# Kernel optimization log

Hardware: AMD Instinct MI355X
Metric: run time of the kernel (lower is better)

## Reference

```python
import jax, jax.numpy as jnp
import numpy as np

T = 1.0  # temperature

def _free_energy(v, W, b, c):
    # v: [B, V]; W: [V, H]; b: [V]; c: [H]
    vW = v @ W                                  # [B, H]
    W_colsum = W.sum(axis=0)                    # [H]
    negF_normal = (v * b).sum(-1) - jax.nn.softplus(vW + c).sum(-1)
    negF_flip = ((1.0 - v) * b).sum(-1) - jax.nn.softplus(W_colsum - vW + c).sum(-1)
    negF = jnp.stack([negF_normal, negF_flip], axis=-1)  # [B, 2]
    return -T * jax.nn.logsumexp(negF / T, axis=-1)      # [B]

def _gibbs_chain(v0, W, b, c, key, k):
    B = v0.shape[0]
    key, k0 = jax.random.split(key)
    u0 = jax.random.bernoulli(k0, 0.5, (B, 1)).astype(v0.dtype)
    b_sum = b.sum()

    def step(carry, _):
        v, u, key = carry
        key, k1, k2, k3 = jax.random.split(key, 4)
        v_branch = u * v + (1.0 - u) * (1.0 - v)
        h = jax.random.bernoulli(k1, jax.nn.sigmoid(v_branch @ W + c)).astype(v.dtype)  # [B,H]
        a = h @ W.T                                                                     # [B,V]
        vb = (v * b).sum(-1)
        va = (v * a).sum(-1)
        dE = -b_sum - a.sum(-1) + 2.0 * vb + 2.0 * va
        u_new = jax.random.bernoulli(k2, jax.nn.sigmoid(dE)).astype(v.dtype)[:, None]
        v_new = jax.random.bernoulli(k3, jax.nn.sigmoid(a + b)).astype(v.dtype)
        v = u_new * v_new + (1.0 - u_new) * (1.0 - v_new)
        return (v, u_new, key), None

    (v_model, _, _), _ = jax.lax.scan(step, (v0, u0, key), None, length=k)
    return v_model

def setup_inputs() -> dict:
    key = jax.random.key(0)
    kv, kw = jax.random.split(key)
    B, V, H = 8192, 1024, 1024
    v_data = jnp.round(jax.random.uniform(kv, (B, V), dtype=jnp.float32))  # binary 0/1
    W = 0.01 * jax.random.normal(kw, (V, H), dtype=jnp.float32)
    b = jnp.zeros((V,), dtype=jnp.float32)
    c = jnp.zeros((H,), dtype=jnp.float32)
    return {"v_data": v_data, "W": W, "b": b, "c": c, "seed": 0}

def reference(v_data, W, b, c, seed):
    K = 10  # Gibbs steps
    key = jax.random.key(seed)
    v_model = _gibbs_chain(v_data, W, b, c, key, K)
    v_model = jax.lax.stop_gradient(v_model)  # .detach() in torch
    loss = _free_energy(v_data, W, b, c).mean() - _free_energy(v_model, W, b, c).mean()
    return loss
```

## Files before the change

kernel.cpp:

```cpp
#include <hip/hip_runtime.h>
#include <hip/hip_bf16.h>
#include <stdint.h>
#include <math.h>


static constexpr int Bn = 8192;
static constexpr int Vn = 1024;
static constexpr int Hn = 1024;
static constexpr int KSTEPS = 10;

typedef _Float16 f16;
typedef f16   f16x4 __attribute__((ext_vector_type(4)));
typedef f16   f16x8 __attribute__((ext_vector_type(8)));
typedef float f32x4 __attribute__((ext_vector_type(4)));

#define GLOBAL_LOAD_LDS16(g, l)                                              \
  __builtin_amdgcn_global_load_lds(                                          \
      (const __attribute__((address_space(1))) uint32_t*)(g),                \
      (__attribute__((address_space(3))) uint32_t*)(l), 16, 0, 0)

__device__ __forceinline__ uint32_t rotl32(uint32_t x, int d) {
  return (x << d) | (x >> (32 - d));
}

__device__ __forceinline__ void tf2x32(uint32_t k0, uint32_t k1,
                                       uint32_t x0, uint32_t x1,
                                       uint32_t& o0, uint32_t& o1) {
  uint32_t k2 = k0 ^ k1 ^ 0x1BD11BDAu;
#define TFR(r) { x0 += x1; x1 = rotl32(x1, (r)); x1 ^= x0; }
  x0 += k0; x1 += k1;
  TFR(13) TFR(15) TFR(26) TFR(6)
  x0 += k1; x1 += k2 + 1u;
  TFR(17) TFR(29) TFR(16) TFR(24)
  x0 += k2; x1 += k0 + 2u;
  TFR(13) TFR(15) TFR(26) TFR(6)
  x0 += k0; x1 += k1 + 3u;
  TFR(17) TFR(29) TFR(16) TFR(24)
  x0 += k1; x1 += k2 + 4u;
  TFR(13) TFR(15) TFR(26) TFR(6)
  x0 += k2; x1 += k0 + 5u;
#undef TFR
  o0 = x0; o1 = x1;
}

__device__ __forceinline__ float rng_u01(uint2 key, uint32_t idx) {
  uint32_t o0, o1;
  tf2x32(key.x, key.y, 0u, idx, o0, o1);
  uint32_t bits = o0 ^ o1;
  return __uint_as_float((bits >> 9) | 0x3F800000u) - 1.0f;
}

__device__ __forceinline__ float bern_fast(float z, float r01) {
  float e = __expf(-z);
  return (__builtin_fmaf(r01, e, r01) < 1.0f) ? 1.f : 0.f;
}
__device__ __forceinline__ float softplus_fast(float x) {
  return fmaxf(x, 0.f) + __logf(1.f + __expf(-fabsf(x)));
}

__global__ void prep_keys(const int* __restrict__ seedp, uint2* __restrict__ keys) {
  if (threadIdx.x != 0 || blockIdx.x != 0) return;
  uint32_t seed = (uint32_t)(*seedp);
  uint2 key = make_uint2(0u, seed);
  uint2 nk, kk;
  tf2x32(key.x, key.y, 0u, 0u, nk.x, nk.y);
  tf2x32(key.x, key.y, 0u, 1u, kk.x, kk.y);
  keys[0] = kk;
  key = nk;
  for (int s = 0; s < KSTEPS; ++s) {
    uint2 t0, t1, t2, t3;
    tf2x32(key.x, key.y, 0u, 0u, t0.x, t0.y);
    tf2x32(key.x, key.y, 0u, 1u, t1.x, t1.y);
    tf2x32(key.x, key.y, 0u, 2u, t2.x, t2.y);
    tf2x32(key.x, key.y, 0u, 3u, t3.x, t3.y);
    key = t0;
    keys[1 + 3*s] = t1;
    keys[2 + 3*s] = t2;
    keys[3 + 3*s] = t3;
  }
}

__global__ __launch_bounds__(256) void colsum_part(
    const float* __restrict__ W, float* __restrict__ part) {
  const int bx = blockIdx.x, t = threadIdx.x;
  float s0 = 0.f, s1 = 0.f, s2 = 0.f, s3 = 0.f;
#pragma unroll
  for (int r = 0; r < 16; ++r) {
    const float* row = W + (size_t)(bx * 16 + r) * Hn;
    s0 += row[t]; s1 += row[t + 256]; s2 += row[t + 512]; s3 += row[t + 768];
  }
  float* p = part + (size_t)bx * Hn;
  p[t] = s0; p[t + 256] = s1; p[t + 512] = s2; p[t + 768] = s3;
}

__global__ __launch_bounds__(256) void colsum_red(
    const float* __restrict__ part, float* __restrict__ cs) {
  const int col = blockIdx.x * 256 + threadIdx.x;
  float s = 0.f;
#pragma unroll
  for (int k = 0; k < 64; ++k) s += part[(size_t)k * Hn + col];
  cs[col] = s;
}

__global__ void bsum_k(const float* __restrict__ bvec, float* __restrict__ bs) {
  __shared__ float sb[4];
  float s = 0.f;
  for (int i = threadIdx.x; i < Vn; i += 256) s += bvec[i];
  for (int off = 32; off > 0; off >>= 1) s += __shfl_down(s, off, 64);
  int wv = threadIdx.x >> 6, ln = threadIdx.x & 63;
  if (ln == 0) sb[wv] = s;
  __syncthreads();
  if (threadIdx.x == 0) bs[0] = sb[0] + sb[1] + sb[2] + sb[3];
}

__global__ __launch_bounds__(256) void cast_W(
    const float* __restrict__ W, f16* __restrict__ Wf, f16* __restrict__ WTf) {
  __shared__ f16 tile[64][65];
  const int j0 = blockIdx.x * 64, i0 = blockIdx.y * 64;
  const int tx = threadIdx.x & 63, tg = threadIdx.x >> 6;
#pragma unroll 4
  for (int rr = 0; rr < 16; ++rr) {
    const int row = tg * 16 + rr;
    float w = W[(size_t)(i0 + row) * Hn + j0 + tx];
    f16 hw = (f16)w;
    Wf[(size_t)(i0 + row) * Hn + j0 + tx] = hw;
    tile[row][tx] = hw;
  }
  __syncthreads();
#pragma unroll 4
  for (int rr = 0; rr < 16; ++rr) {
    const int row = tg * 16 + rr;
    WTf[(size_t)(j0 + row) * Vn + i0 + tx] = tile[tx][row];
  }
}

__global__ void u0_init(const uint2* __restrict__ keys, float* __restrict__ u0) {
  int b = blockIdx.x * 256 + threadIdx.x;
  float r01 = rng_u01(keys[0], (uint32_t)b);
  u0[b] = (r01 < 0.5f) ? 1.f : 0.f;
}

__global__ __launch_bounds__(256) void cast_vx(
    const float* __restrict__ vd, const float* __restrict__ u0,
    const float* __restrict__ bvec, f16* __restrict__ x,
    float* __restrict__ pXB0) {
  const int row = blockIdx.x;
  const int t = threadIdx.x;
  const float uo = u0[row];
  const float4 d  = ((const float4*)(vd + (size_t)row * Vn))[t];
  const float4 bv = ((const float4*)bvec)[t];
  float xv[4] = { d.x, d.y, d.z, d.w };
  if (uo <= 0.5f) { xv[0]=1.f-xv[0]; xv[1]=1.f-xv[1]; xv[2]=1.f-xv[2]; xv[3]=1.f-xv[3]; }
  f16x4 o = { (f16)xv[0], (f16)xv[1], (f16)xv[2], (f16)xv[3] };
  *(f16x4*)(x + (size_t)row * Vn + t * 4) = o;
  float xb = xv[0]*bv.x + xv[1]*bv.y + xv[2]*bv.z + xv[3]*bv.w;
#pragma unroll
  for (int m = 1; m < 8; m <<= 1) xb += __shfl_xor(xb, m, 64);
  if ((t & 7) == 0) pXB0[(size_t)row * 32 + (t >> 3)] = xb;
}

template <int EPI>
__global__ __launch_bounds__(256, 2) void gemm_s(
    const f16* __restrict__ A, const f16* __restrict__ Bm,
    f16* __restrict__ outH, f16* __restrict__ xnew,
    const float* __restrict__ bvec, const float* __restrict__ cvec,
    const float* __restrict__ colsum,
    float* __restrict__ pA, float* __restrict__ pXA, float* __restrict__ pXBn,
    float* __restrict__ pSA, float* __restrict__ pSB,
    const uint2* __restrict__ keys, int keyIdx)
{
  constexpr int N = 1024, K = 1024, BK = 64;
  __shared__ alignas(16) f16 As[128 * BK];
  __shared__ alignas(16) f16 Bs[128 * BK];

  const int t = threadIdx.x, wave = t >> 6, lane = t & 63;
  const int l15 = lane & 15, quad = lane >> 4;
  const int m0 = blockIdx.x * 128, n0 = blockIdx.y * 128;
  const int wm = (wave >> 1) * 64, wn = (wave & 1) * 64;

  const int rbase = lane >> 3;
  const int gch   = (lane & 7) ^ rbase;
  const f16* gA = A  + (size_t)(m0 + wave * 32 + rbase) * K + gch * 8;
  const f16* gB = Bm + (size_t)(n0 + wave * 32 + rbase) * K + gch * 8;
  f16* lA = As + wave * 32 * BK;
  f16* lB = Bs + wave * 32 * BK;

  const int swz = l15 & 7;
  const int oA  = (wm + l15) * BK;
  const int oB  = (wn + l15) * BK;

  f32x4 acc[4][4] = {};

  for (int k0 = 0; k0 < K; k0 += BK) {
#pragma unroll
    for (int i = 0; i < 4; ++i) {
      GLOBAL_LOAD_LDS16(gA + k0 + i * 8 * K, lA + i * 8 * BK);
      GLOBAL_LOAD_LDS16(gB + k0 + i * 8 * K, lB + i * 8 * BK);
    }
    __syncthreads();

#pragma unroll
    for (int kc = 0; kc < 2; ++kc) {
      const int fc = ((kc * 4 + quad) ^ swz) * 8;
      f16x8 af[4], bf[4];
#pragma unroll
      for (int i = 0; i < 4; ++i) {
        af[i] = *(const f16x8*)(&As[oA + i * 16 * BK + fc]);
        bf[i] = *(const f16x8*)(&Bs[oB + i * 16 * BK + fc]);
      }
#pragma unroll
      for (int mt = 0; mt < 4; ++mt)
#pragma unroll
        for (int nt = 0; nt < 4; ++nt)
          acc[mt][nt] = __builtin_amdgcn_mfma_f32_16x16x32_f16(af[mt], bf[nt], acc[mt][nt], 0, 0, 0);
    }
    __syncthreads();
  }

  const int slotBase = blockIdx.y * 4 + (wave & 1) * 2;

  if constexpr (EPI == 1 || EPI == 2) {
    const uint2 key = keys[keyIdx];
    float csv[4], cvv[4];
#pragma unroll
    for (int nt = 0; nt < 4; ++nt) {
      const int gn = n0 + wn + nt * 16 + l15;
      csv[nt] = colsum[gn];
      cvv[nt] = cvec[gn];
    }
#pragma unroll
    for (int mt = 0; mt < 4; ++mt)
#pragma unroll
      for (int r = 0; r < 4; ++r) {
        const int gm = m0 + wm + mt * 16 + quad * 4 + r;
#pragma unroll
        for (int p = 0; p < 2; ++p) {
          float pa = 0.f, pxa = 0.f, sa = 0.f, sb = 0.f;
#pragma unroll
          for (int q = 0; q < 2; ++q) {
            const int nt = p * 2 + q;
            const int gn = n0 + wn + nt * 16 + l15;
            const float val = acc[mt][nt][r];
            float r01 = rng_u01(key, (uint32_t)(gm * N + gn));
            float hq  = bern_fast(val + cvv[nt], r01);
            outH[(size_t)gm * N + gn] = (f16)hq;
            pa  += hq * csv[nt];
            pxa += hq * val;
            if constexpr (EPI == 2) {
              sa += softplus_fast(val + cvv[nt]);
              sb += softplus_fast(csv[nt] - val + cvv[nt]);
            }
          }
#pragma unroll
          for (int m = 1; m < 16; m <<= 1) {
            pa  += __shfl_xor(pa,  m, 64);
            pxa += __shfl_xor(pxa, m, 64);
            if constexpr (EPI == 2) {
              sa += __shfl_xor(sa, m, 64);
              sb += __shfl_xor(sb, m, 64);
            }
          }
          if (l15 == 0) {
            pA [(size_t)gm * 32 + slotBase + p] = pa;
            pXA[(size_t)gm * 32 + slotBase + p] = pxa;
            if constexpr (EPI == 2) {
              pSA[(size_t)gm * 32 + slotBase + p] = sa;
              pSB[(size_t)gm * 32 + slotBase + p] = sb;
            }
          }
        }
      }
  } else if constexpr (EPI == 3) {
    const uint2 key = keys[keyIdx];
    float bb[4];
#pragma unroll
    for (int nt = 0; nt < 4; ++nt) bb[nt] = bvec[n0 + wn + nt * 16 + l15];
#pragma unroll
    for (int mt = 0; mt < 4; ++mt)
#pragma unroll
      for (int r = 0; r < 4; ++r) {
        const int gm = m0 + wm + mt * 16 + quad * 4 + r;
#pragma unroll
        for (int p = 0; p < 2; ++p) {
          float pxb = 0.f;
#pragma unroll
          for (int q = 0; q < 2; ++q) {
            const int nt = p * 2 + q;
            const int gn = n0 + wn + nt * 16 + l15;
            const float aval = acc[mt][nt][r];
            float r01 = rng_u01(key, (uint32_t)(gm * N + gn));
            float xq  = bern_fast(aval + bb[nt], r01);
            xnew[(size_t)gm * N + gn] = (f16)xq;
            pxb += xq * bb[nt];
          }
#pragma unroll
          for (int m = 1; m < 16; m <<= 1) pxb += __shfl_xor(pxb, m, 64);
          if (l15 == 0) pXBn[(size_t)gm * 32 + slotBase + p] = pxb;
        }
      }
  } else {
    float csv[4], cvv[4];
#pragma unroll
    for (int nt = 0; nt < 4; ++nt) {
      const int gn = n0 + wn + nt * 16 + l15;
      csv[nt] = colsum[gn];
      cvv[nt] = cvec[gn];
    }
#pragma unroll
    for (int mt = 0; mt < 4; ++mt)
#pragma unroll
      for (int r = 0; r < 4; ++r) {
        const int gm = m0 + wm + mt * 16 + quad * 4 + r;
#pragma unroll
        for (int p = 0; p < 2; ++p) {
          float sa = 0.f, sb = 0.f;
#pragma unroll
          for (int q = 0; q < 2; ++q) {
            const int nt = p * 2 + q;
            const float val = acc[mt][nt][r];
            sa += softplus_fast(val + cvv[nt]);
            sb += softplus_fast(csv[nt] - val + cvv[nt]);
          }
#pragma unroll
          for (int m = 1; m < 16; m <<= 1) {
            sa += __shfl_xor(sa, m, 64);
            sb += __shfl_xor(sb, m, 64);
          }
          if (l15 == 0) {
            pSA[(size_t)gm * 32 + slotBase + p] = sa;
            pSB[(size_t)gm * 32 + slotBase + p] = sb;
          }
        }
      }
  }
}

__global__ __launch_bounds__(256) void u_chain(
    const float* __restrict__ pA, const float* __restrict__ pXA,
    const float* __restrict__ pXB, const float* __restrict__ bsum,
    const uint2* __restrict__ keys, const float* __restrict__ u0,
    float* __restrict__ uF)
{
  const int t = threadIdx.x, wave = t >> 6, lane = t & 63;
  const int r2 = lane >> 5, slot = lane & 31;
  const int row = blockIdx.x * 8 + wave * 2 + r2;
  const float bs = bsum[0];
  float uo = u0[row];
  for (int s = 0; s < KSTEPS; ++s) {
    const size_t o = (size_t)s * 32 * Bn + (size_t)row * 32 + slot;
    float sa  = pA [o];
    float sxa = pXA[o];
    float sxb = pXB[o];
#pragma unroll
    for (int m = 1; m < 32; m <<= 1) {
      sa  += __shfl_xor(sa,  m, 64);
      sxa += __shfl_xor(sxa, m, 64);
      sxb += __shfl_xor(sxb, m, 64);
    }
    const float va = (uo > 0.5f) ? sxa : sa - sxa;
    const float vb = (uo > 0.5f) ? sxb : bs - sxb;
    const float dE = -bs - sa + 2.f * vb + 2.f * va;
    uo = bern_fast(dE, rng_u01(keys[2 + 3 * s], (uint32_t)row));
  }
  if (slot == 0) uF[row] = uo;
}

__device__ __forceinline__ float fe_eval(float SA, float SB, float xb,
                                         float uo, float bs) {
  float S1 = (uo > 0.5f) ? SA : SB;
  float S2 = (uo > 0.5f) ? SB : SA;
  float vb = (uo > 0.5f) ? xb : bs - xb;
  float negn = vb - S1;
  float negf = (bs - vb) - S2;
  float mx = fmaxf(negn, negf);
  return -(mx + logf(expf(negn - mx) + expf(negf - mx)));
}

__global__ __launch_bounds__(256) void fe_finish(
    const float* __restrict__ SA0, const float* __restrict__ SB0,
    const float* __restrict__ xb0,
    const float* __restrict__ SAF, const float* __restrict__ SBF,
    const float* __restrict__ xbF,
    const float* __restrict__ u0, const float* __restrict__ uF,
    const float* __restrict__ bsum,
    float* __restrict__ Fd, float* __restrict__ Fm)
{
  const int t = threadIdx.x, wave = t >> 6, lane = t & 63;
  const int r2 = lane >> 5, slot = lane & 31;
  const int row = blockIdx.x * 8 + wave * 2 + r2;
  const size_t o = (size_t)row * 32 + slot;
  const float bs = bsum[0];
  float a0 = SA0[o], b0 = SB0[o], x0 = xb0[o];
  float aF = SAF[o], bF = SBF[o], xF = xbF[o];
#pragma unroll
  for (int m = 1; m < 32; m <<= 1) {
    a0 += __shfl_xor(a0, m, 64);  b0 += __shfl_xor(b0, m, 64);
    x0 += __shfl_xor(x0, m, 64);  aF += __shfl_xor(aF, m, 64);
    bF += __shfl_xor(bF, m, 64);  xF += __shfl_xor(xF, m, 64);
  }
  if (slot == 0) {
    Fd[row] = fe_eval(a0, b0, x0, u0[row], bs);
    Fm[row] = fe_eval(aF, bF, xF, uF[row], bs);
  }
}

__global__ __launch_bounds__(256) void finalize_k(
    const float* __restrict__ Fd, const float* __restrict__ Fm, float* __restrict__ out)
{
  __shared__ double sb[8];
  double sd = 0.0, sm = 0.0;
  for (int i = threadIdx.x; i < Bn; i += 256) { sd += (double)Fd[i]; sm += (double)Fm[i]; }
  for (int off = 32; off > 0; off >>= 1) { sd += __shfl_down(sd, off, 64); sm += __shfl_down(sm, off, 64); }
  const int wv = threadIdx.x >> 6, ln = threadIdx.x & 63;
  if (ln == 0) { sb[wv] = sd; sb[4 + wv] = sm; }
  __syncthreads();
  if (threadIdx.x == 0) {
    sd = sb[0] + sb[1] + sb[2] + sb[3];
    sm = sb[4] + sb[5] + sb[6] + sb[7];
    out[0] = (float)((sd - sm) / (double)Bn);
  }
}

extern "C" void kernel_launch(void* const* d_in, const int* in_sizes, int n_in,
                              void* d_out, int out_size, void* d_ws, size_t ws_size,
                              hipStream_t stream) {
  const float* v_data = (const float*)d_in[0];
  const float* W      = (const float*)d_in[1];
  const float* bvec   = (const float*)d_in[2];
  const float* cvec   = (const float*)d_in[3];
  const int*   seedp  = (const int*)d_in[4];
  float* out = (float*)d_out;

  char* ws = (char*)d_ws;
  size_t off = 0;
  auto alloc = [&](size_t bytes) -> void* {
    void* p = ws + off;
    off += (bytes + 255) & ~(size_t)255;
    return p;
  };
  f16*   xb0  = (f16*)alloc((size_t)Bn * Vn * 2);
  f16*   xb1  = (f16*)alloc((size_t)Bn * Vn * 2);
  f16*   h    = (f16*)alloc((size_t)Bn * Hn * 2);
  f16*   Wf   = (f16*)alloc((size_t)Vn * Hn * 2);
  f16*   WTf  = (f16*)alloc((size_t)Vn * Hn * 2);
  float* cpart  = (float*)alloc(64 * Hn * 4);
  float* colsum = (float*)alloc(Hn * 4);
  float* bsum   = (float*)alloc(256);
  uint2* keys   = (uint2*)alloc(64 * sizeof(uint2));
  float* u0     = (float*)alloc(Bn * 4);
  float* uF     = (float*)alloc(Bn * 4);
  float* pA     = (float*)alloc((size_t)KSTEPS * 32 * Bn * 4);
  float* pXA    = (float*)alloc((size_t)KSTEPS * 32 * Bn * 4);
  float* pXB    = (float*)alloc((size_t)(KSTEPS + 1) * 32 * Bn * 4);
  float* SA0    = (float*)alloc((size_t)32 * Bn * 4);
  float* SB0    = (float*)alloc((size_t)32 * Bn * 4);
  float* SAF    = (float*)alloc((size_t)32 * Bn * 4);
  float* SBF    = (float*)alloc((size_t)32 * Bn * 4);
  float* Fd     = (float*)alloc(Bn * 4);
  float* Fm     = (float*)alloc(Bn * 4);
  (void)ws_size; (void)in_sizes; (void)n_in; (void)out_size;

  prep_keys<<<1, 64, 0, stream>>>(seedp, keys);
  colsum_part<<<64, 256, 0, stream>>>(W, cpart);
  colsum_red<<<4, 256, 0, stream>>>(cpart, colsum);
  bsum_k<<<1, 256, 0, stream>>>(bvec, bsum);
  cast_W<<<dim3(Hn / 64, Vn / 64), 256, 0, stream>>>(W, Wf, WTf);
  u0_init<<<Bn / 256, 256, 0, stream>>>(keys, u0);
  cast_vx<<<Bn, 256, 0, stream>>>(v_data, u0, bvec, xb0, pXB);

  dim3 gg(Bn / 128, Hn / 128);
  f16* xs[2] = { xb0, xb1 };
  const size_t SL = (size_t)32 * Bn;

  for (int s = 0; s < KSTEPS; ++s) {
    if (s == 0) {
      gemm_s<2><<<gg, 256, 0, stream>>>(xs[0], WTf, h, nullptr, nullptr, cvec,
                                        colsum, pA, pXA, nullptr, SA0, SB0,
                                        keys, 1);
    } else {
      gemm_s<1><<<gg, 256, 0, stream>>>(xs[s & 1], WTf, h, nullptr, nullptr, cvec,
                                        colsum, pA + (size_t)s * SL,
                                        pXA + (size_t)s * SL, nullptr,
                                        nullptr, nullptr, keys, 1 + 3 * s);
    }
    gemm_s<3><<<gg, 256, 0, stream>>>(h, Wf, nullptr, xs[(s + 1) & 1], bvec,
                                      nullptr, nullptr, nullptr, nullptr,
                                      pXB + (size_t)(s + 1) * SL,
                                      nullptr, nullptr, keys, 3 + 3 * s);
  }

  gemm_s<4><<<gg, 256, 0, stream>>>(xs[KSTEPS & 1], WTf, nullptr, nullptr,
                                    nullptr, cvec, colsum, nullptr, nullptr,
                                    nullptr, SAF, SBF, keys, 0);

  u_chain<<<Bn / 8, 256, 0, stream>>>(pA, pXA, pXB, bsum, keys, u0, uF);
  fe_finish<<<Bn / 8, 256, 0, stream>>>(SA0, SB0, pXB,
                                        SAF, SBF, pXB + (size_t)KSTEPS * SL,
                                        u0, uF, bsum, Fd, Fm);
  finalize_k<<<1, 256, 0, stream>>>(Fd, Fm, out);
}
```

Before: 955.8 us.

## Interleave Threefry RNG generation with GEMM K-loop to overlap ALU with MFMA

Moves the per-element Threefry random number generation out of the GEMM epilogue and into the main K loop, generating four values per iteration while the tile loads are in flight. The random values are kept in a 64-entry register array and consumed by the Bernoulli sampling epilogue. The aim is to hide the integer RNG cost behind memory and MFMA latency. In exchange it raises register pressure, which can lower occupancy or cause spills. It also fully unrolls the loop and hardcodes K to 1024 with BK of 64, and routes the RNG through a noinline helper that adds call overhead.

```diff
diff --git a/kernel.cpp b/kernel.cpp
--- a/kernel.cpp
+++ b/kernel.cpp
@@ -48,6 +48,17 @@
   tf2x32(key.x, key.y, 0u, idx, o0, o1);
   uint32_t bits = o0 ^ o1;
   return __uint_as_float((bits >> 9) | 0x3F800000u) - 1.0f;
+}
+
+__device__ __attribute__((noinline)) float4 rng4_u01(uint2 key, uint32_t i0,
+                                                     uint32_t i1, uint32_t i2,
+                                                     uint32_t i3) {
+  float4 r;
+  r.x = rng_u01(key, i0);
+  r.y = rng_u01(key, i1);
+  r.z = rng_u01(key, i2);
+  r.w = rng_u01(key, i3);
+  return r;
 }
 
 __device__ __forceinline__ float bern_fast(float z, float r01) {
@@ -189,13 +200,35 @@
   const int oA  = (wm + l15) * BK;
   const int oB  = (wn + l15) * BK;
 
+  uint2 key = make_uint2(0u, 0u);
+  if constexpr (EPI != 4) key = keys[keyIdx];
+
   f32x4 acc[4][4] = {};
-
-  for (int k0 = 0; k0 < K; k0 += BK) {
+  float r01v[64];
+
+#pragma unroll 16
+  for (int ki = 0; ki < 16; ++ki) {
+    const int k0 = ki * 64;
 #pragma unroll
     for (int i = 0; i < 4; ++i) {
       GLOBAL_LOAD_LDS16(gA + k0 + i * 8 * K, lA + i * 8 * BK);
       GLOBAL_LOAD_LDS16(gB + k0 + i * 8 * K, lB + i * 8 * BK);
+    }
+    if constexpr (EPI != 4) {
+      uint32_t idx[4];
+#pragma unroll
+      for (int j = 0; j < 4; ++j) {
+        const int e  = ki * 4 + j;
+        const int mt = e >> 4, r = (e >> 2) & 3, nt = e & 3;
+        const int gm = m0 + wm + mt * 16 + quad * 4 + r;
+        const int gn = n0 + wn + nt * 16 + l15;
+        idx[j] = (uint32_t)(gm * N + gn);
+      }
+      float4 rv = rng4_u01(key, idx[0], idx[1], idx[2], idx[3]);
+      r01v[ki * 4 + 0] = rv.x;
+      r01v[ki * 4 + 1] = rv.y;
+      r01v[ki * 4 + 2] = rv.z;
+      r01v[ki * 4 + 3] = rv.w;
     }
     __syncthreads();
 
@@ -220,7 +253,6 @@
   const int slotBase = blockIdx.y * 4 + (wave & 1) * 2;
 
   if constexpr (EPI == 1 || EPI == 2) {
-    const uint2 key = keys[keyIdx];
     float csv[4], cvv[4];
 #pragma unroll
     for (int nt = 0; nt < 4; ++nt) {
@@ -241,7 +273,7 @@
             const int nt = p * 2 + q;
             const int gn = n0 + wn + nt * 16 + l15;
             const float val = acc[mt][nt][r];
-            float r01 = rng_u01(key, (uint32_t)(gm * N + gn));
+            const float r01 = r01v[mt * 16 + r * 4 + nt];
             float hq  = bern_fast(val + cvv[nt], r01);
             outH[(size_t)gm * N + gn] = (f16)hq;
             pa  += hq * csv[nt];
@@ -271,7 +303,6 @@
         }
       }
   } else if constexpr (EPI == 3) {
-    const uint2 key = keys[keyIdx];
     float bb[4];
 #pragma unroll
     for (int nt = 0; nt < 4; ++nt) bb[nt] = bvec[n0 + wn + nt * 16 + l15];
@@ -288,7 +319,7 @@
             const int nt = p * 2 + q;
             const int gn = n0 + wn + nt * 16 + l15;
             const float aval = acc[mt][nt][r];
-            float r01 = rng_u01(key, (uint32_t)(gm * N + gn));
+            const float r01 = r01v[mt * 16 + r * 4 + nt];
             float xq  = bern_fast(aval + bb[nt], r01);
             xnew[(size_t)gm * N + gn] = (f16)xq;
             pxb += xq * bb[nt];
```

Result: no change. 950.6 us (-0.5%).

## Load GEMM MFMA fragments directly from global memory and reduce with DPP

Applied to the files above, without the earlier changes.

The GEMM no longer stages A and B tiles through LDS with global_load_lds and barriers. Each wave now reads its 16-byte MFMA fragments straight from global memory inside a fully unrolled K loop, which removes the shared-memory traffic and the __syncthreads pairs. The 16-lane epilogue reductions switch from shfl_xor to DPP quad_perm and mirror adds, and the launch-bounds occupancy hint is dropped. The trade-off is that tiles shared between waves are now fetched more than once and the strided 16-byte loads are less coalesced, so the kernel leans more on L1/L2 bandwidth and register pressure.

```diff
diff --git a/kernel.cpp b/kernel.cpp
--- a/kernel.cpp
+++ b/kernel.cpp
@@ -13,11 +13,6 @@
 typedef f16   f16x4 __attribute__((ext_vector_type(4)));
 typedef f16   f16x8 __attribute__((ext_vector_type(8)));
 typedef float f32x4 __attribute__((ext_vector_type(4)));
-
-#define GLOBAL_LOAD_LDS16(g, l)                                              \
-  __builtin_amdgcn_global_load_lds(                                          \
-      (const __attribute__((address_space(1))) uint32_t*)(g),                \
-      (__attribute__((address_space(3))) uint32_t*)(l), 16, 0, 0)
 
 __device__ __forceinline__ uint32_t rotl32(uint32_t x, int d) {
   return (x << d) | (x >> (32 - d));
@@ -56,6 +51,19 @@
 }
 __device__ __forceinline__ float softplus_fast(float x) {
   return fmaxf(x, 0.f) + __logf(1.f + __expf(-fabsf(x)));
+}
+
+template <int CTRL>
+__device__ __forceinline__ float dpp_add16(float v) {
+  int x = __builtin_amdgcn_update_dpp(0, __float_as_int(v), CTRL, 0xF, 0xF, true);
+  return v + __int_as_float(x);
+}
+__device__ __forceinline__ float red16(float v) {
+  v = dpp_add16<0xB1>(v);
+  v = dpp_add16<0x4E>(v);
+  v = dpp_add16<0x141>(v);
+  v = dpp_add16<0x140>(v);
+  return v;
 }
 
 __global__ void prep_keys(const int* __restrict__ seedp, uint2* __restrict__ keys) {
@@ -160,7 +168,7 @@
 }
 
 template <int EPI>
-__global__ __launch_bounds__(256, 2) void gemm_s(
+__global__ __launch_bounds__(256) void gemm_s(
     const f16* __restrict__ A, const f16* __restrict__ Bm,
     f16* __restrict__ outH, f16* __restrict__ xnew,
     const float* __restrict__ bvec, const float* __restrict__ cvec,
@@ -169,58 +177,48 @@
     float* __restrict__ pSA, float* __restrict__ pSB,
     const uint2* __restrict__ keys, int keyIdx)
 {
-  constexpr int N = 1024, K = 1024, BK = 64;
-  __shared__ alignas(16) f16 As[128 * BK];
-  __shared__ alignas(16) f16 Bs[128 * BK];
+  constexpr int N = 1024, K = 1024;
 
   const int t = threadIdx.x, wave = t >> 6, lane = t & 63;
   const int l15 = lane & 15, quad = lane >> 4;
   const int m0 = blockIdx.x * 128, n0 = blockIdx.y * 128;
   const int wm = (wave >> 1) * 64, wn = (wave & 1) * 64;
 
-  const int rbase = lane >> 3;
-  const int gch   = (lane & 7) ^ rbase;
-  const f16* gA = A  + (size_t)(m0 + wave * 32 + rbase) * K + gch * 8;
-  const f16* gB = Bm + (size_t)(n0 + wave * 32 + rbase) * K + gch * 8;
-  f16* lA = As + wave * 32 * BK;
-  f16* lB = Bs + wave * 32 * BK;
-
-  const int swz = l15 & 7;
-  const int oA  = (wm + l15) * BK;
-  const int oB  = (wn + l15) * BK;
+  const f16* pa[4];
+  const f16* pb[4];
+#pragma unroll
+  for (int i = 0; i < 4; ++i) {
+    pa[i] = A  + (size_t)(m0 + wm + i * 16 + l15) * K + quad * 8;
+    pb[i] = Bm + (size_t)(n0 + wn + i * 16 + l15) * K + quad * 8;
+  }
 
   f32x4 acc[4][4] = {};
 
-  for (int k0 = 0; k0 < K; k0 += BK) {
-#pragma unroll
-    for (int i = 0; i < 4; ++i) {
-      GLOBAL_LOAD_LDS16(gA + k0 + i * 8 * K, lA + i * 8 * BK);
-      GLOBAL_LOAD_LDS16(gB + k0 + i * 8 * K, lB + i * 8 * BK);
-    }
-    __syncthreads();
-
-#pragma unroll
-    for (int kc = 0; kc < 2; ++kc) {
-      const int fc = ((kc * 4 + quad) ^ swz) * 8;
-      f16x8 af[4], bf[4];
+#pragma unroll
+  for (int ki = 0; ki < 16; ++ki) {
+    const int k0 = ki * 64;
+    f16x8 af[2][4], bf[2][4];
+#pragma unroll
+    for (int kc = 0; kc < 2; ++kc)
 #pragma unroll
       for (int i = 0; i < 4; ++i) {
-        af[i] = *(const f16x8*)(&As[oA + i * 16 * BK + fc]);
-        bf[i] = *(const f16x8*)(&Bs[oB + i * 16 * BK + fc]);
+        af[kc][i] = *(const f16x8*)(pa[i] + k0 + kc * 32);
+        bf[kc][i] = *(const f16x8*)(pb[i] + k0 + kc * 32);
       }
 #pragma unroll
+    for (int kc = 0; kc < 2; ++kc)
+#pragma unroll
       for (int mt = 0; mt < 4; ++mt)
 #pragma unroll
         for (int nt = 0; nt < 4; ++nt)
-          acc[mt][nt] = __builtin_amdgcn_mfma_f32_16x16x32_f16(af[mt], bf[nt], acc[mt][nt], 0, 0, 0);
-    }
-    __syncthreads();
+          acc[mt][nt] = __builtin_amdgcn_mfma_f32_16x16x32_f16(af[kc][mt], bf[kc][nt], acc[mt][nt], 0, 0, 0);
   }
 
   const int slotBase = blockIdx.y * 4 + (wave & 1) * 2;
+  uint2 key = make_uint2(0u, 0u);
+  if constexpr (EPI != 4) key = keys[keyIdx];
 
   if constexpr (EPI == 1 || EPI == 2) {
-    const uint2 key = keys[keyIdx];
     float csv[4], cvv[4];
 #pragma unroll
     for (int nt = 0; nt < 4; ++nt) {
@@ -235,7 +233,7 @@
         const int gm = m0 + wm + mt * 16 + quad * 4 + r;
 #pragma unroll
         for (int p = 0; p < 2; ++p) {
-          float pa = 0.f, pxa = 0.f, sa = 0.f, sb = 0.f;
+          float pa2 = 0.f, pxa = 0.f, sa = 0.f, sb = 0.f;
 #pragma unroll
           for (int q = 0; q < 2; ++q) {
             const int nt = p * 2 + q;
@@ -244,24 +242,21 @@
             float r01 = rng_u01(key, (uint32_t)(gm * N + gn));
             float hq  = bern_fast(val + cvv[nt], r01);
             outH[(size_t)gm * N + gn] = (f16)hq;
-            pa  += hq * csv[nt];
+            pa2 += hq * csv[nt];
             pxa += hq * val;
             if constexpr (EPI == 2) {
               sa += softplus_fast(val + cvv[nt]);
               sb += softplus_fast(csv[nt] - val + cvv[nt]);
             }
           }
-#pragma unroll
-          for (int m = 1; m < 16; m <<= 1) {
-            pa  += __shfl_xor(pa,  m, 64);
-            pxa += __shfl_xor(pxa, m, 64);
-            if constexpr (EPI == 2) {
-              sa += __shfl_xor(sa, m, 64);
-              sb += __shfl_xor(sb, m, 64);
-            }
+          pa2 = red16(pa2);
+          pxa = red16(pxa);
+          if constexpr (EPI == 2) {
+            sa = red16(sa);
+            sb = red16(sb);
           }
           if (l15 == 0) {
-            pA [(size_t)gm * 32 + slotBase + p] = pa;
+            pA [(size_t)gm * 32 + slotBase + p] = pa2;
             pXA[(size_t)gm * 32 + slotBase + p] = pxa;
             if constexpr (EPI == 2) {
               pSA[(size_t)gm * 32 + slotBase + p] = sa;
@@ -271,7 +266,6 @@
         }
       }
   } else if constexpr (EPI == 3) {
-    const uint2 key = keys[keyIdx];
     float bb[4];
 #pragma unroll
     for (int nt = 0; nt < 4; ++nt) bb[nt] = bvec[n0 + wn + nt * 16 + l15];
@@ -293,8 +287,7 @@
             xnew[(size_t)gm * N + gn] = (f16)xq;
             pxb += xq * bb[nt];
           }
-#pragma unroll
-          for (int m = 1; m < 16; m <<= 1) pxb += __shfl_xor(pxb, m, 64);
+          pxb = red16(pxb);
           if (l15 == 0) pXBn[(size_t)gm * 32 + slotBase + p] = pxb;
         }
       }
@@ -321,11 +314,8 @@
             sa += softplus_fast(val + cvv[nt]);
             sb += softplus_fast(csv[nt] - val + cvv[nt]);
           }
-#pragma unroll
-          for (int m = 1; m < 16; m <<= 1) {
-            sa += __shfl_xor(sa, m, 64);
-            sb += __shfl_xor(sb, m, 64);
-          }
+          sa = red16(sa);
+          sb = red16(sb);
           if (l15 == 0) {
             pSA[(size_t)gm * 32 + slotBase + p] = sa;
             pSB[(size_t)gm * 32 + slotBase + p] = sb;
```

After: 1.757 ms. 83.9% more time.
